# Performance work log

Measured on AMD Instinct MI355X. Metric: run time of the kernel, lower is better.

The kernel has to match this reference:

```python
import math
import jax, jax.numpy as jnp
import numpy as np

B_, H_, L_, N_ = 64, 256, 1024, 64  # batch, n_feat, n_embd(=seq len), complex state modes (d_state=128 -> 64 conj pairs)


def setup_inputs() -> dict:
    key = jax.random.key(0)
    ks = jax.random.split(key, 12)
    x = jax.random.normal(ks[0], (B_, H_, L_), jnp.float32)
    t = jax.random.randint(ks[1], (B_,), 0, 1000)
    # AdaLayerNorm linear: n_embd -> 2*n_embd
    ada_w = jax.random.normal(ks[2], (2 * L_, L_), jnp.float32) * 0.02
    ada_b = jnp.zeros((2 * L_,), jnp.float32)
    # S4Layer prenorm (LayerNorm over n_feat, affine)
    norm_w = jnp.ones((H_,), jnp.float32)
    norm_b = jnp.zeros((H_,), jnp.float32)
    # S4D-style diagonal SSM parameters
    log_dt = math.log(0.001) + jax.random.uniform(ks[3], (H_,), jnp.float32) * (math.log(0.1) - math.log(0.001))
    A_re = jnp.full((H_, N_), math.log(0.5), jnp.float32)            # A_real = -exp(A_re) = -0.5
    A_im = jnp.ones((H_, 1), jnp.float32) * (math.pi * jnp.arange(N_, dtype=jnp.float32))[None, :]
    C_re = jax.random.normal(ks[4], (2, H_, N_), jnp.float32) * (N_ ** -0.5)  # 2 channels: bidirectional
    C_im = jax.random.normal(ks[5], (2, H_, N_), jnp.float32) * (N_ ** -0.5)
    D = jax.random.normal(ks[6], (H_,), jnp.float32)
    out_w = jax.random.normal(ks[7], (H_, H_), jnp.float32) * (H_ ** -0.5)   # S4 output 1x1 conv
    out_b = jnp.zeros((H_,), jnp.float32)
    lin1_w = jax.random.normal(ks[8], (H_, H_), jnp.float32) * (H_ ** -0.5)
    lin1_b = jnp.zeros((H_,), jnp.float32)
    lin2_w = jax.random.normal(ks[9], (H_, H_), jnp.float32) * (H_ ** -0.5)
    lin2_b = jnp.zeros((H_,), jnp.float32)
    return dict(x=x, t=t, ada_w=ada_w, ada_b=ada_b, norm_w=norm_w, norm_b=norm_b,
                log_dt=log_dt, A_re=A_re, A_im=A_im, C_re=C_re, C_im=C_im, D=D,
                out_w=out_w, out_b=out_b, lin1_w=lin1_w, lin1_b=lin1_b,
                lin2_w=lin2_w, lin2_b=lin2_b)


def _ln(v):
    m = v.mean(-1, keepdims=True)
    s = v.var(-1, keepdims=True)
    return (v - m) * jax.lax.rsqrt(s + 1e-5)


def _forward(t, x, ada_w, ada_b, norm_w, norm_b, log_dt, A_re, A_im, C_re, C_im, D,
             out_w, out_b, lin1_w, lin1_b, lin2_w, lin2_b):
    B, H, L = x.shape
    # ---- AdaLayerNorm over last dim (n_embd = L) ----
    half = L // 2
    freqs = jnp.exp(jnp.arange(half, dtype=jnp.float32) * (-math.log(10000.0) / (half - 1)))
    emb = t.astype(jnp.float32)[:, None] * freqs[None, :]
    emb = jnp.concatenate([jnp.sin(emb), jnp.cos(emb)], axis=-1)           # (B, L)
    emb = jax.nn.silu(emb) @ ada_w.T + ada_b                                # (B, 2L)
    scale, shift = jnp.split(emb[:, None, :], 2, axis=2)                    # (B,1,L)
    x = _ln(x) * (1.0 + scale) + shift                                      # (B,H,L)
    # ---- S4Layer: prenorm over channels ----
    z = (_ln(x.transpose(0, 2, 1)) * norm_w + norm_b).transpose(0, 2, 1)    # (B,H,L)
    # ---- S4 (diagonal SSM) bidirectional FFT convolution ----
    dt = jnp.exp(log_dt)                                                    # (H,)
    A = -jnp.exp(A_re) + 1j * A_im                                          # (H,N)
    dtA = dt[:, None] * A
    dA = jnp.exp(dtA)
    C = (C_re + 1j * C_im) * ((dA - 1.0) / A)                               # ZOH-discretized (2,H,N)
    vand = jnp.exp(dtA[:, :, None] * jnp.arange(L, dtype=jnp.float32))      # (H,N,L)
    K = 2.0 * jnp.real(jnp.einsum('chn,hnl->chl', C, vand))                 # (2,H,L)
    k = jnp.pad(K[0], ((0, 0), (0, L))) + jnp.pad(K[1][:, ::-1], ((0, 0), (L, 0)))  # (H,2L)
    n = 2 * L
    y = jnp.fft.irfft(jnp.fft.rfft(z, n=n) * jnp.fft.rfft(k, n=n), n=n)[..., :L]
    y = y + D[:, None] * z
    y = jax.nn.gelu(y, approximate=False)
    y = jnp.einsum('oi,bil->bol', out_w, y) + out_b[None, :, None]          # S4 output 1x1 conv
    x2 = y + x                                                              # residual
    # ---- gated output ----
    g = jnp.tanh(x2) * jax.nn.sigmoid(x2)
    out1 = jnp.einsum('oi,bil->bol', lin1_w, g) + lin1_b[None, :, None] + x
    out2 = jnp.einsum('oi,bil->bol', lin2_w, g) + lin2_b[None, :, None]
    return (out1, out2)


def reference(x, t, ada_w, ada_b, norm_w, norm_b, log_dt, A_re, A_im, C_re, C_im, D,
              out_w, out_b, lin1_w, lin1_b, lin2_w, lin2_b):
    return _forward(t, x, ada_w, ada_b, norm_w, norm_b, log_dt, A_re, A_im, C_re, C_im,
                    D, out_w, out_b, lin1_w, lin1_b, lin2_w, lin2_b)
```

## Files before the change

kernel.cpp:

```cpp
#include <hip/hip_runtime.h>
#include <math.h>

#define Bq 64
#define Hq 256
#define Lq 1024
#define HLq (Hq*Lq)
#define BHLq (Bq*Hq*Lq)
#define HNq (Hq*64)

typedef __attribute__((ext_vector_type(8))) short bf16x8;
typedef __attribute__((ext_vector_type(4))) float f32x4;

__device__ __forceinline__ float sigmoidf_(float x){ return 1.f/(1.f+expf(-x)); }
__device__ __forceinline__ unsigned short f2bf(float f){
  unsigned u = __float_as_uint(f);
  u += 0x7FFF + ((u>>16)&1);
  return (unsigned short)(u>>16);
}
__device__ __forceinline__ float bf2f(unsigned short h){ return __uint_as_float(((unsigned)h)<<16); }

__global__ __launch_bounds__(256) void k_ada2(const int* __restrict__ tptr,
        const float* __restrict__ ada_w, float* __restrict__ Part){
  __shared__ float Es[64][68];
  __shared__ float Ws[64][68];
  const int tid = threadIdx.x;
  const int o0 = blockIdx.x * 64;
  const int kc = blockIdx.y;
  const int k0 = kc * 64;
  const float ci = -logf(10000.f) / 511.f;
  #pragma unroll
  for (int it = 0; it < 4; ++it){
    int fidx = it*256 + tid;
    int row = fidx >> 4;
    int c4  = fidx & 15;
    float tb = (float)tptr[row];
    float4 v;
    float* vp = &v.x;
    #pragma unroll
    for (int q = 0; q < 4; ++q){
      int k = k0 + c4*4 + q;
      float f = expf(ci * (float)(k & 511));
      float arg = tb * f;
      float s = (k < 512) ? sinf(arg) : cosf(arg);
      vp[q] = s * sigmoidf_(s);
    }
    *(float4*)&Es[row][c4*4] = v;
  }
  #pragma unroll
  for (int it = 0; it < 4; ++it){
    int fidx = it*256 + tid;
    int row = fidx >> 4;
    int c4  = fidx & 15;
    *(float4*)&Ws[row][c4*4] = *(const float4*)(ada_w + (size_t)(o0+row)*1024 + k0 + c4*4);
  }
  __syncthreads();
  float acc[4][4] = {};
  #pragma unroll
  for (int ks = 0; ks < 16; ++ks){
    int k = ks*4;
    float4 ev[4], wv[4];
    #pragma unroll
    for (int i=0;i<4;++i) ev[i] = *(const float4*)&Es[(tid>>4) + 16*i][k];
    #pragma unroll
    for (int j=0;j<4;++j) wv[j] = *(const float4*)&Ws[(tid&15) + 16*j][k];
    #pragma unroll
    for (int i=0;i<4;++i)
      #pragma unroll
      for (int j=0;j<4;++j)
        acc[i][j] += ev[i].x*wv[j].x + ev[i].y*wv[j].y + ev[i].z*wv[j].z + ev[i].w*wv[j].w;
  }
  float* pbase = Part + (size_t)kc*131072 + o0;
  #pragma unroll
  for (int i=0;i<4;++i){
    int b = (tid>>4) + 16*i;
    #pragma unroll
    for (int j=0;j<4;++j){
      int o = (tid&15) + 16*j;
      pbase[(size_t)b*2048 + o] = acc[i][j];
    }
  }
}

__global__ void k_red(const float* __restrict__ Part, const float* __restrict__ ada_b,
                      float* __restrict__ scsh){
  int idx = blockIdx.x*256 + threadIdx.x;
  float4 s = ((const float4*)ada_b)[idx & 511];
  #pragma unroll
  for (int p = 0; p < 16; ++p){
    float4 u = ((const float4*)Part)[p*32768 + idx];
    s.x += u.x; s.y += u.y; s.z += u.z; s.w += u.w;
  }
  ((float4*)scsh)[idx] = s;
}

__global__ void k_adaln(const float* __restrict__ x, const float* __restrict__ scsh,
                        float* __restrict__ A){
  const int bid = blockIdx.x;
  const int b = bid >> 8;
  const int tid = threadIdx.x;
  const float4* row = (const float4*)(x + (size_t)bid*1024);
  float4 v = row[tid];
  float s = v.x+v.y+v.z+v.w;
  float ss = v.x*v.x+v.y*v.y+v.z*v.z+v.w*v.w;
  #pragma unroll
  for (int off=32; off; off>>=1){ s += __shfl_xor(s,off); ss += __shfl_xor(ss,off); }
  __shared__ float rs_[4], rss_[4];
  int lane = tid & 63, w = tid >> 6;
  if (!lane){ rs_[w]=s; rss_[w]=ss; }
  __syncthreads();
  s  = rs_[0]+rs_[1]+rs_[2]+rs_[3];
  ss = rss_[0]+rss_[1]+rss_[2]+rss_[3];
  float mean = s * (1.f/1024.f);
  float var  = ss*(1.f/1024.f) - mean*mean;
  float rstd = rsqrtf(var + 1e-5f);
  float4 sc = ((const float4*)(scsh + b*2048))[tid];
  float4 sh = ((const float4*)(scsh + b*2048 + 1024))[tid];
  float4 o;
  o.x = (v.x-mean)*rstd*(1.f+sc.x) + sh.x;
  o.y = (v.y-mean)*rstd*(1.f+sc.y) + sh.y;
  o.z = (v.z-mean)*rstd*(1.f+sc.z) + sh.z;
  o.w = (v.w-mean)*rstd*(1.f+sc.w) + sh.w;
  ((float4*)(A + (size_t)bid*1024))[tid] = o;
}

__global__ void k_chln(const float* __restrict__ A, const float* __restrict__ nw,
                       const float* __restrict__ nb, unsigned short* __restrict__ Zb){
  const int b = blockIdx.y;
  const int l = blockIdx.x*256 + threadIdx.x;
  const float* base = A + (size_t)b*HLq + l;
  float s=0.f, ss=0.f;
  for (int h=0; h<256; ++h){ float v = base[h*1024]; s+=v; ss+=v*v; }
  float mean = s*(1.f/256.f);
  float var  = ss*(1.f/256.f) - mean*mean;
  float rstd = rsqrtf(var+1e-5f);
  unsigned short* zb = Zb + (size_t)b*HLq + l;
  for (int h=0; h<256; ++h){
    float v = base[h*1024];
    zb[h*1024] = f2bf((v-mean)*rstd*nw[h] + nb[h]);
  }
}

__global__ void k_ssmk(const float* __restrict__ log_dt, const float* __restrict__ A_re,
                       const float* __restrict__ A_im, const float* __restrict__ C_re,
                       const float* __restrict__ C_im, float* __restrict__ Kbuf){
  const int h = blockIdx.y;
  const int tid = threadIdx.x;
  __shared__ float dre[64], dim_[64], c0r[64], c0i[64], c1r[64], c1i[64];
  if (tid < 64){
    int n = tid;
    float dt = expf(log_dt[h]);
    float Ar = -expf(A_re[h*64+n]);
    float Ai = A_im[h*64+n];
    float dr = dt*Ar, di = dt*Ai;
    float er = expf(dr);
    float dAr = er*cosf(di), dAi = er*sinf(di);
    float den = Ar*Ar + Ai*Ai;
    float nr = dAr - 1.f, ni = dAi;
    float qr = (nr*Ar + ni*Ai)/den;
    float qi = (ni*Ar - nr*Ai)/den;
    float C0r = C_re[h*64+n],       C0i = C_im[h*64+n];
    float C1r = C_re[HNq + h*64+n], C1i = C_im[HNq + h*64+n];
    c0r[n] = C0r*qr - C0i*qi; c0i[n] = C0r*qi + C0i*qr;
    c1r[n] = C1r*qr - C1i*qi; c1i[n] = C1r*qi + C1i*qr;
    dre[n] = dr; dim_[n] = di;
  }
  __syncthreads();
  int l = blockIdx.x*256 + tid;
  float lf = (float)l;
  float a0=0.f, a1=0.f;
  for (int n=0;n<64;++n){
    float e  = expf(lf*dre[n]);
    float ph = lf*dim_[n];
    float wr = e*cosf(ph), wi = e*sinf(ph);
    a0 += c0r[n]*wr - c0i[n]*wi;
    a1 += c1r[n]*wr - c1i[n]*wi;
  }
  Kbuf[h*1024 + l]       = 2.f*a0;
  Kbuf[HLq + h*1024 + l] = 2.f*a1;
}

__global__ __launch_bounds__(256,2) void k_conv(const unsigned short* __restrict__ Zb,
        const float* __restrict__ Kbuf, const float* __restrict__ Dp,
        unsigned short* __restrict__ Cb){
  __shared__ unsigned short kcopy[8][2056];
  __shared__ unsigned short As[64][136];
  const int tid = threadIdx.x;
  const int h  = blockIdx.y;
  const int l0 = blockIdx.x * 512;
  const float* K0 = Kbuf + h*1024;
  const float* K1 = Kbuf + HLq + h*1024;
  for (int idx = tid; idx < 8*2056; idx += 256){
    int s = idx / 2056;
    int i = idx - s*2056;
    int q = 2046 - i - s;
    float v = 0.f;
    if (q >= 0) v = (q >= 1023) ? K0[q-1023] : K1[1022-q];
    kcopy[s][i] = f2bf(v);
  }
  const int lane = tid & 63;
  const int w    = tid >> 6;
  const int ln   = lane & 15;
  const int quad = lane >> 4;
  int kofs[8];
  #pragma unroll
  for (int nt=0; nt<8; ++nt){
    int l = l0 + w*128 + nt*16 + ln;
    int d = 1023 - l;
    int s = d & 7;
    kofs[nt] = s*2056 + (d - s) + quad*8;
  }
  const unsigned short* kbase = &kcopy[0][0];
  f32x4 acc[4][8] = {};
  for (int c = 0; c < 8; ++c){
    __syncthreads();
    #pragma unroll
    for (int pass = 0; pass < 4; ++pass){
      int b = pass*16 + (tid>>4);
      int col = (tid & 15)*8;
      *(uint4*)&As[b][col] = *(const uint4*)(Zb + ((size_t)b*256 + h)*1024 + c*128 + col);
    }
    __syncthreads();
    #pragma unroll
    for (int ks = 0; ks < 4; ++ks){
      int kk = ks*32 + quad*8;
      bf16x8 af[4];
      #pragma unroll
      for (int mt=0; mt<4; ++mt) af[mt] = *(const bf16x8*)&As[mt*16+ln][kk];
      int jb = c*128 + ks*32;
      bf16x8 bv[8];
      #pragma unroll
      for (int nt=0; nt<8; ++nt) bv[nt] = *(const bf16x8*)(kbase + kofs[nt] + jb);
      #pragma unroll
      for (int mt=0; mt<4; ++mt)
        #pragma unroll
        for (int nt=0; nt<8; ++nt)
          acc[mt][nt] = __builtin_amdgcn_mfma_f32_16x16x32_bf16(af[mt], bv[nt], acc[mt][nt], 0,0,0);
    }
  }
  float Dh = Dp[h];
  #pragma unroll
  for (int mt=0; mt<4; ++mt){
    #pragma unroll
    for (int reg=0; reg<4; ++reg){
      int b = mt*16 + quad*4 + reg;
      const unsigned short* zrow = Zb + ((size_t)b*256+h)*1024;
      unsigned short* crow = Cb + ((size_t)b*256+h)*1024;
      #pragma unroll
      for (int nt=0; nt<8; ++nt){
        int l = l0 + w*128 + nt*16 + ln;
        float y = acc[mt][nt][reg] + Dh*bf2f(zrow[l]);
        float g = 0.5f*y*(1.f + erff(y*0.70710678118f));
        crow[l] = f2bf(g);
      }
    }
  }
}

__global__ __launch_bounds__(256,2) void k_gate(const unsigned short* __restrict__ U,
        const float* __restrict__ W, const float* __restrict__ bias,
        const float* __restrict__ Ax, unsigned short* __restrict__ G){
  __shared__ unsigned short Ws[64][72];
  __shared__ unsigned short Us[256][72];
  const int tid = threadIdx.x;
  const int l0 = blockIdx.x * 256;
  const int o0 = blockIdx.y * 64;
  const int b  = blockIdx.z;
  const int lane = tid & 63, w = tid>>6, ln = lane&15, quad = lane>>4;
  f32x4 acc[4][4] = {};
  for (int ch = 0; ch < 4; ++ch){
    int ic0 = ch*64;
    __syncthreads();
    {
      int o = tid & 63;
      int i = (tid >> 6) * 16;
      const float* wsrc = W + (size_t)(o0+o)*256 + ic0 + i;
      unsigned pk[8];
      #pragma unroll
      for (int r=0;r<8;++r) pk[r] = (unsigned)f2bf(wsrc[2*r]) | ((unsigned)f2bf(wsrc[2*r+1])<<16);
      uint4* dst = (uint4*)&Ws[o][i];
      dst[0] = make_uint4(pk[0],pk[1],pk[2],pk[3]);
      dst[1] = make_uint4(pk[4],pk[5],pk[6],pk[7]);
    }
    #pragma unroll
    for (int it = 0; it < 16; ++it){
      int i4 = (tid>>6) + 4*(it&3);
      int l  = (it>>2)*64 + (tid&63);
      const unsigned short* usrc = U + ((size_t)b*256 + ic0 + i4*4)*1024 + l0 + l;
      unsigned short e0 = usrc[0], e1 = usrc[1024], e2 = usrc[2048], e3 = usrc[3072];
      uint2 val; val.x = (unsigned)e0 | ((unsigned)e1<<16); val.y = (unsigned)e2 | ((unsigned)e3<<16);
      *(uint2*)&Us[l][i4*4] = val;
    }
    __syncthreads();
    #pragma unroll
    for (int ks = 0; ks < 2; ++ks){
      int kk = ks*32 + quad*8;
      bf16x8 af[4], bv[4];
      #pragma unroll
      for (int mt=0;mt<4;++mt) af[mt] = *(const bf16x8*)&Ws[mt*16+ln][kk];
      #pragma unroll
      for (int nt=0;nt<4;++nt) bv[nt] = *(const bf16x8*)&Us[w*64+nt*16+ln][kk];
      #pragma unroll
      for (int mt=0;mt<4;++mt)
        #pragma unroll
        for (int nt=0;nt<4;++nt)
          acc[mt][nt] = __builtin_amdgcn_mfma_f32_16x16x32_bf16(af[mt], bv[nt], acc[mt][nt],0,0,0);
    }
  }
  #pragma unroll
  for (int mt=0;mt<4;++mt){
    #pragma unroll
    for (int reg=0;reg<4;++reg){
      int o = o0 + mt*16 + quad*4 + reg;
      float bo = bias[o];
      const float* arow = Ax + ((size_t)b*256 + o)*1024;
      unsigned short* grow = G + ((size_t)b*256 + o)*1024;
      #pragma unroll
      for (int nt=0;nt<4;++nt){
        int l = l0 + w*64 + nt*16 + ln;
        float v = acc[mt][nt][reg] + bo + arow[l];
        float g = tanhf(v)*sigmoidf_(v);
        grow[l] = f2bf(g);
      }
    }
  }
}

__global__ __launch_bounds__(256,2) void k_out(const unsigned short* __restrict__ G,
        const float* __restrict__ W1, const float* __restrict__ b1,
        const float* __restrict__ W2, const float* __restrict__ b2,
        const float* __restrict__ Ax, float* __restrict__ out){
  __shared__ unsigned short W1s[64][72];
  __shared__ unsigned short W2s[64][72];
  __shared__ unsigned short Us[256][72];
  const int tid = threadIdx.x;
  const int l0 = blockIdx.x * 256;
  const int o0 = blockIdx.y * 64;
  const int b  = blockIdx.z;
  const int lane = tid & 63, w = tid>>6, ln = lane&15, quad = lane>>4;
  f32x4 acc1[4][4] = {};
  f32x4 acc2[4][4] = {};
  for (int ch = 0; ch < 4; ++ch){
    int ic0 = ch*64;
    __syncthreads();
    {
      int o = tid & 63;
      int i = (tid >> 6) * 16;
      const float* w1src = W1 + (size_t)(o0+o)*256 + ic0 + i;
      const float* w2src = W2 + (size_t)(o0+o)*256 + ic0 + i;
      unsigned pk[8];
      #pragma unroll
      for (int r=0;r<8;++r) pk[r] = (unsigned)f2bf(w1src[2*r]) | ((unsigned)f2bf(w1src[2*r+1])<<16);
      uint4* dst1 = (uint4*)&W1s[o][i];
      dst1[0] = make_uint4(pk[0],pk[1],pk[2],pk[3]);
      dst1[1] = make_uint4(pk[4],pk[5],pk[6],pk[7]);
      #pragma unroll
      for (int r=0;r<8;++r) pk[r] = (unsigned)f2bf(w2src[2*r]) | ((unsigned)f2bf(w2src[2*r+1])<<16);
      uint4* dst2 = (uint4*)&W2s[o][i];
      dst2[0] = make_uint4(pk[0],pk[1],pk[2],pk[3]);
      dst2[1] = make_uint4(pk[4],pk[5],pk[6],pk[7]);
    }
    #pragma unroll
    for (int it = 0; it < 16; ++it){
      int i4 = (tid>>6) + 4*(it&3);
      int l  = (it>>2)*64 + (tid&63);
      const unsigned short* usrc = G + ((size_t)b*256 + ic0 + i4*4)*1024 + l0 + l;
      unsigned short e0 = usrc[0], e1 = usrc[1024], e2 = usrc[2048], e3 = usrc[3072];
      uint2 val; val.x = (unsigned)e0 | ((unsigned)e1<<16); val.y = (unsigned)e2 | ((unsigned)e3<<16);
      *(uint2*)&Us[l][i4*4] = val;
    }
    __syncthreads();
    #pragma unroll
    for (int ks = 0; ks < 2; ++ks){
      int kk = ks*32 + quad*8;
      bf16x8 bv[4];
      #pragma unroll
      for (int nt=0;nt<4;++nt) bv[nt] = *(const bf16x8*)&Us[w*64+nt*16+ln][kk];
      #pragma unroll
      for (int mt=0;mt<4;++mt){
        bf16x8 a1 = *(const bf16x8*)&W1s[mt*16+ln][kk];
        #pragma unroll
        for (int nt=0;nt<4;++nt)
          acc1[mt][nt] = __builtin_amdgcn_mfma_f32_16x16x32_bf16(a1, bv[nt], acc1[mt][nt],0,0,0);
      }
      #pragma unroll
      for (int mt=0;mt<4;++mt){
        bf16x8 a2 = *(const bf16x8*)&W2s[mt*16+ln][kk];
        #pragma unroll
        for (int nt=0;nt<4;++nt)
          acc2[mt][nt] = __builtin_amdgcn_mfma_f32_16x16x32_bf16(a2, bv[nt], acc2[mt][nt],0,0,0);
      }
    }
  }
  #pragma unroll
  for (int mt=0;mt<4;++mt){
    #pragma unroll
    for (int reg=0;reg<4;++reg){
      int o = o0 + mt*16 + quad*4 + reg;
      float bo1 = b1[o], bo2 = b2[o];
      const float* arow = Ax + ((size_t)b*256 + o)*1024;
      float* o1row = out + ((size_t)b*256 + o)*1024;
      float* o2row = o1row + BHLq;
      #pragma unroll
      for (int nt=0;nt<4;++nt){
        int l = l0 + w*64 + nt*16 + ln;
        o1row[l] = acc1[mt][nt][reg] + bo1 + arow[l];
        o2row[l] = acc2[mt][nt][reg] + bo2;
      }
    }
  }
}

extern "C" void kernel_launch(void* const* d_in, const int* in_sizes, int n_in,
                              void* d_out, int out_size, void* d_ws, size_t ws_size,
                              hipStream_t stream){
  const float* x      = (const float*)d_in[0];
  const int*   t      = (const int*)  d_in[1];
  const float* ada_w  = (const float*)d_in[2];
  const float* ada_b  = (const float*)d_in[3];
  const float* norm_w = (const float*)d_in[4];
  const float* norm_b = (const float*)d_in[5];
  const float* log_dt = (const float*)d_in[6];
  const float* A_re   = (const float*)d_in[7];
  const float* A_im   = (const float*)d_in[8];
  const float* C_re   = (const float*)d_in[9];
  const float* C_im   = (const float*)d_in[10];
  const float* Dp     = (const float*)d_in[11];
  const float* out_w  = (const float*)d_in[12];
  const float* out_b  = (const float*)d_in[13];
  const float* lin1_w = (const float*)d_in[14];
  const float* lin1_b = (const float*)d_in[15];
  const float* lin2_w = (const float*)d_in[16];
  const float* lin2_b = (const float*)d_in[17];

  float* Ax            = (float*)d_ws;
  unsigned short* Zb   = (unsigned short*)(Ax + BHLq);
  unsigned short* Cb   = Zb + BHLq;
  float* Kbuf          = (float*)(Cb + BHLq);
  float* Part          = Kbuf + 2*HLq;
  float* scsh          = Part + 16*64*2048;
  unsigned short* Gb   = Zb;
  float* out           = (float*)d_out;

  k_ada2  <<<dim3(32, 16), 256, 0, stream>>>(t, ada_w, Part);
  k_red   <<<128, 256, 0, stream>>>(Part, ada_b, scsh);
  k_adaln <<<Bq*Hq, 256, 0, stream>>>(x, scsh, Ax);
  k_chln  <<<dim3(4, Bq), 256, 0, stream>>>(Ax, norm_w, norm_b, Zb);
  k_ssmk  <<<dim3(4, Hq), 256, 0, stream>>>(log_dt, A_re, A_im, C_re, C_im, Kbuf);
  k_conv  <<<dim3(2, Hq), 256, 0, stream>>>(Zb, Kbuf, Dp, Cb);
  k_gate  <<<dim3(4, 4, Bq), 256, 0, stream>>>(Cb, out_w, out_b, Ax, Gb);
  k_out   <<<dim3(4, 4, Bq), 256, 0, stream>>>(Gb, lin1_w, lin1_b, lin2_w, lin2_b, Ax, out);
}
```

Before: 532.1 us.

## Fuse gate and output 1x1 convs into one kernel with pre-converted bf16 weights

```diff
diff --git a/kernel.cpp b/kernel.cpp
--- a/kernel.cpp
+++ b/kernel.cpp
@@ -91,6 +91,18 @@
     s.x += u.x; s.y += u.y; s.z += u.z; s.w += u.w;
   }
   ((float4*)scsh)[idx] = s;
+}
+
+__global__ void k_wcvt(const float* __restrict__ w0, const float* __restrict__ w1,
+                       const float* __restrict__ w2, unsigned short* __restrict__ wb){
+  int idx = blockIdx.x*256 + threadIdx.x;
+  const float* src = (idx < 16384) ? w0 : ((idx < 32768) ? w1 : w2);
+  int loc = idx & 16383;
+  float4 v = ((const float4*)src)[loc];
+  uint2 pk;
+  pk.x = (unsigned)f2bf(v.x) | ((unsigned)f2bf(v.y)<<16);
+  pk.y = (unsigned)f2bf(v.z) | ((unsigned)f2bf(v.w)<<16);
+  ((uint2*)wb)[idx] = pk;
 }
 
 __global__ void k_adaln(const float* __restrict__ x, const float* __restrict__ scsh,
@@ -256,154 +268,106 @@
   }
 }
 
-__global__ __launch_bounds__(256,2) void k_gate(const unsigned short* __restrict__ U,
-        const float* __restrict__ W, const float* __restrict__ bias,
-        const float* __restrict__ Ax, unsigned short* __restrict__ G){
-  __shared__ unsigned short Ws[64][72];
-  __shared__ unsigned short Us[256][72];
+__global__ __launch_bounds__(512,2) void k_fuse(const unsigned short* __restrict__ U,
+        const unsigned short* __restrict__ Wob, const float* __restrict__ out_b,
+        const unsigned short* __restrict__ W1b, const float* __restrict__ b1,
+        const unsigned short* __restrict__ W2b, const float* __restrict__ b2,
+        const float* __restrict__ Ax, float* __restrict__ out){
+  __shared__ unsigned short Us[64][280];
+  __shared__ unsigned short Gs[64][280];
   const int tid = threadIdx.x;
-  const int l0 = blockIdx.x * 256;
-  const int o0 = blockIdx.y * 64;
-  const int b  = blockIdx.z;
-  const int lane = tid & 63, w = tid>>6, ln = lane&15, quad = lane>>4;
-  f32x4 acc[4][4] = {};
-  for (int ch = 0; ch < 4; ++ch){
-    int ic0 = ch*64;
-    __syncthreads();
-    {
-      int o = tid & 63;
-      int i = (tid >> 6) * 16;
-      const float* wsrc = W + (size_t)(o0+o)*256 + ic0 + i;
-      unsigned pk[8];
-      #pragma unroll
-      for (int r=0;r<8;++r) pk[r] = (unsigned)f2bf(wsrc[2*r]) | ((unsigned)f2bf(wsrc[2*r+1])<<16);
-      uint4* dst = (uint4*)&Ws[o][i];
-      dst[0] = make_uint4(pk[0],pk[1],pk[2],pk[3]);
-      dst[1] = make_uint4(pk[4],pk[5],pk[6],pk[7]);
-    }
-    #pragma unroll
-    for (int it = 0; it < 16; ++it){
-      int i4 = (tid>>6) + 4*(it&3);
-      int l  = (it>>2)*64 + (tid&63);
-      const unsigned short* usrc = U + ((size_t)b*256 + ic0 + i4*4)*1024 + l0 + l;
+  const int l0 = blockIdx.x * 64;
+  const int b  = blockIdx.y;
+  const int lane = tid & 63, w = tid >> 6, ln = lane & 15, quad = lane >> 4;
+  {
+    int l   = tid & 63;
+    int grp = tid >> 6;
+    #pragma unroll
+    for (int it = 0; it < 8; ++it){
+      int i4 = it*8 + grp;
+      const unsigned short* usrc = U + ((size_t)b*256 + i4*4)*1024 + l0 + l;
       unsigned short e0 = usrc[0], e1 = usrc[1024], e2 = usrc[2048], e3 = usrc[3072];
       uint2 val; val.x = (unsigned)e0 | ((unsigned)e1<<16); val.y = (unsigned)e2 | ((unsigned)e3<<16);
       *(uint2*)&Us[l][i4*4] = val;
     }
-    __syncthreads();
-    #pragma unroll
-    for (int ks = 0; ks < 2; ++ks){
-      int kk = ks*32 + quad*8;
-      bf16x8 af[4], bv[4];
-      #pragma unroll
-      for (int mt=0;mt<4;++mt) af[mt] = *(const bf16x8*)&Ws[mt*16+ln][kk];
-      #pragma unroll
-      for (int nt=0;nt<4;++nt) bv[nt] = *(const bf16x8*)&Us[w*64+nt*16+ln][kk];
-      #pragma unroll
-      for (int mt=0;mt<4;++mt)
-        #pragma unroll
-        for (int nt=0;nt<4;++nt)
-          acc[mt][nt] = __builtin_amdgcn_mfma_f32_16x16x32_bf16(af[mt], bv[nt], acc[mt][nt],0,0,0);
-    }
-  }
-  #pragma unroll
-  for (int mt=0;mt<4;++mt){
+  }
+  __syncthreads();
+  f32x4 acc[2][4] = {};
+  #pragma unroll
+  for (int ks = 0; ks < 8; ++ks){
+    int kk = ks*32 + quad*8;
+    bf16x8 af[2], bv[4];
+    #pragma unroll
+    for (int mt=0;mt<2;++mt) af[mt] = *(const bf16x8*)(Wob + (size_t)(w*32+mt*16+ln)*256 + kk);
+    #pragma unroll
+    for (int nt=0;nt<4;++nt) bv[nt] = *(const bf16x8*)&Us[nt*16+ln][kk];
+    #pragma unroll
+    for (int mt=0;mt<2;++mt)
+      #pragma unroll
+      for (int nt=0;nt<4;++nt)
+        acc[mt][nt] = __builtin_amdgcn_mfma_f32_16x16x32_bf16(af[mt], bv[nt], acc[mt][nt],0,0,0);
+  }
+  float axv[2][4][4];
+  #pragma unroll
+  for (int mt=0;mt<2;++mt){
     #pragma unroll
     for (int reg=0;reg<4;++reg){
-      int o = o0 + mt*16 + quad*4 + reg;
-      float bo = bias[o];
-      const float* arow = Ax + ((size_t)b*256 + o)*1024;
-      unsigned short* grow = G + ((size_t)b*256 + o)*1024;
+      int o = w*32 + mt*16 + quad*4 + reg;
+      float bo = out_b[o];
+      const float* arow = Ax + ((size_t)b*256 + o)*1024 + l0;
       #pragma unroll
       for (int nt=0;nt<4;++nt){
-        int l = l0 + w*64 + nt*16 + ln;
-        float v = acc[mt][nt][reg] + bo + arow[l];
-        float g = tanhf(v)*sigmoidf_(v);
-        grow[l] = f2bf(g);
+        int l = nt*16 + ln;
+        float a = arow[l];
+        axv[mt][nt][reg] = a;
+        float v = acc[mt][nt][reg] + bo + a;
+        acc[mt][nt][reg] = tanhf(v)*sigmoidf_(v);
       }
     }
   }
-}
-
-__global__ __launch_bounds__(256,2) void k_out(const unsigned short* __restrict__ G,
-        const float* __restrict__ W1, const float* __restrict__ b1,
-        const float* __restrict__ W2, const float* __restrict__ b2,
-        const float* __restrict__ Ax, float* __restrict__ out){
-  __shared__ unsigned short W1s[64][72];
-  __shared__ unsigned short W2s[64][72];
-  __shared__ unsigned short Us[256][72];
-  const int tid = threadIdx.x;
-  const int l0 = blockIdx.x * 256;
-  const int o0 = blockIdx.y * 64;
-  const int b  = blockIdx.z;
-  const int lane = tid & 63, w = tid>>6, ln = lane&15, quad = lane>>4;
-  f32x4 acc1[4][4] = {};
-  f32x4 acc2[4][4] = {};
-  for (int ch = 0; ch < 4; ++ch){
-    int ic0 = ch*64;
-    __syncthreads();
-    {
-      int o = tid & 63;
-      int i = (tid >> 6) * 16;
-      const float* w1src = W1 + (size_t)(o0+o)*256 + ic0 + i;
-      const float* w2src = W2 + (size_t)(o0+o)*256 + ic0 + i;
-      unsigned pk[8];
-      #pragma unroll
-      for (int r=0;r<8;++r) pk[r] = (unsigned)f2bf(w1src[2*r]) | ((unsigned)f2bf(w1src[2*r+1])<<16);
-      uint4* dst1 = (uint4*)&W1s[o][i];
-      dst1[0] = make_uint4(pk[0],pk[1],pk[2],pk[3]);
-      dst1[1] = make_uint4(pk[4],pk[5],pk[6],pk[7]);
-      #pragma unroll
-      for (int r=0;r<8;++r) pk[r] = (unsigned)f2bf(w2src[2*r]) | ((unsigned)f2bf(w2src[2*r+1])<<16);
-      uint4* dst2 = (uint4*)&W2s[o][i];
-      dst2[0] = make_uint4(pk[0],pk[1],pk[2],pk[3]);
-      dst2[1] = make_uint4(pk[4],pk[5],pk[6],pk[7]);
-    }
-    #pragma unroll
-    for (int it = 0; it < 16; ++it){
-      int i4 = (tid>>6) + 4*(it&3);
-      int l  = (it>>2)*64 + (tid&63);
-      const unsigned short* usrc = G + ((size_t)b*256 + ic0 + i4*4)*1024 + l0 + l;
-      unsigned short e0 = usrc[0], e1 = usrc[1024], e2 = usrc[2048], e3 = usrc[3072];
-      uint2 val; val.x = (unsigned)e0 | ((unsigned)e1<<16); val.y = (unsigned)e2 | ((unsigned)e3<<16);
-      *(uint2*)&Us[l][i4*4] = val;
-    }
-    __syncthreads();
-    #pragma unroll
-    for (int ks = 0; ks < 2; ++ks){
-      int kk = ks*32 + quad*8;
-      bf16x8 bv[4];
-      #pragma unroll
-      for (int nt=0;nt<4;++nt) bv[nt] = *(const bf16x8*)&Us[w*64+nt*16+ln][kk];
-      #pragma unroll
-      for (int mt=0;mt<4;++mt){
-        bf16x8 a1 = *(const bf16x8*)&W1s[mt*16+ln][kk];
-        #pragma unroll
-        for (int nt=0;nt<4;++nt)
-          acc1[mt][nt] = __builtin_amdgcn_mfma_f32_16x16x32_bf16(a1, bv[nt], acc1[mt][nt],0,0,0);
-      }
-      #pragma unroll
-      for (int mt=0;mt<4;++mt){
-        bf16x8 a2 = *(const bf16x8*)&W2s[mt*16+ln][kk];
-        #pragma unroll
-        for (int nt=0;nt<4;++nt)
-          acc2[mt][nt] = __builtin_amdgcn_mfma_f32_16x16x32_bf16(a2, bv[nt], acc2[mt][nt],0,0,0);
-      }
-    }
-  }
-  #pragma unroll
-  for (int mt=0;mt<4;++mt){
+  #pragma unroll
+  for (int mt=0;mt<2;++mt){
+    int ob = w*32 + mt*16 + quad*4;
+    #pragma unroll
+    for (int nt=0;nt<4;++nt){
+      uint2 pk;
+      pk.x = (unsigned)f2bf(acc[mt][nt][0]) | ((unsigned)f2bf(acc[mt][nt][1])<<16);
+      pk.y = (unsigned)f2bf(acc[mt][nt][2]) | ((unsigned)f2bf(acc[mt][nt][3])<<16);
+      *(uint2*)&Gs[nt*16+ln][ob] = pk;
+    }
+  }
+  __syncthreads();
+  f32x4 acc1[2][4] = {}, acc2[2][4] = {};
+  #pragma unroll
+  for (int ks = 0; ks < 8; ++ks){
+    int kk = ks*32 + quad*8;
+    bf16x8 bv[4];
+    #pragma unroll
+    for (int nt=0;nt<4;++nt) bv[nt] = *(const bf16x8*)&Gs[nt*16+ln][kk];
+    #pragma unroll
+    for (int mt=0;mt<2;++mt){
+      bf16x8 a1 = *(const bf16x8*)(W1b + (size_t)(w*32+mt*16+ln)*256 + kk);
+      #pragma unroll
+      for (int nt=0;nt<4;++nt)
+        acc1[mt][nt] = __builtin_amdgcn_mfma_f32_16x16x32_bf16(a1, bv[nt], acc1[mt][nt],0,0,0);
+      bf16x8 a2 = *(const bf16x8*)(W2b + (size_t)(w*32+mt*16+ln)*256 + kk);
+      #pragma unroll
+      for (int nt=0;nt<4;++nt)
+        acc2[mt][nt] = __builtin_amdgcn_mfma_f32_16x16x32_bf16(a2, bv[nt], acc2[mt][nt],0,0,0);
+    }
+  }
+  #pragma unroll
+  for (int mt=0;mt<2;++mt){
     #pragma unroll
     for (int reg=0;reg<4;++reg){
-      int o = o0 + mt*16 + quad*4 + reg;
+      int o = w*32 + mt*16 + quad*4 + reg;
       float bo1 = b1[o], bo2 = b2[o];
-      const float* arow = Ax + ((size_t)b*256 + o)*1024;
-      float* o1row = out + ((size_t)b*256 + o)*1024;
+      float* o1row = out + ((size_t)b*256 + o)*1024 + l0;
       float* o2row = o1row + BHLq;
       #pragma unroll
       for (int nt=0;nt<4;++nt){
-        int l = l0 + w*64 + nt*16 + ln;
-        o1row[l] = acc1[mt][nt][reg] + bo1 + arow[l];
+        int l = nt*16 + ln;
+        o1row[l] = acc1[mt][nt][reg] + bo1 + axv[mt][nt][reg];
         o2row[l] = acc2[mt][nt][reg] + bo2;
       }
     }
@@ -438,15 +402,16 @@
   float* Kbuf          = (float*)(Cb + BHLq);
   float* Part          = Kbuf + 2*HLq;
   float* scsh          = Part + 16*64*2048;
-  unsigned short* Gb   = Zb;
+  unsigned short* wb   = (unsigned short*)(scsh + 64*2048);
   float* out           = (float*)d_out;
 
+  k_wcvt  <<<192, 256, 0, stream>>>(out_w, lin1_w, lin2_w, wb);
   k_ada2  <<<dim3(32, 16), 256, 0, stream>>>(t, ada_w, Part);
   k_red   <<<128, 256, 0, stream>>>(Part, ada_b, scsh);
   k_adaln <<<Bq*Hq, 256, 0, stream>>>(x, scsh, Ax);
   k_chln  <<<dim3(4, Bq), 256, 0, stream>>>(Ax, norm_w, norm_b, Zb);
   k_ssmk  <<<dim3(4, Hq), 256, 0, stream>>>(log_dt, A_re, A_im, C_re, C_im, Kbuf);
   k_conv  <<<dim3(2, Hq), 256, 0, stream>>>(Zb, Kbuf, Dp, Cb);
-  k_gate  <<<dim3(4, 4, Bq), 256, 0, stream>>>(Cb, out_w, out_b, Ax, Gb);
-  k_out   <<<dim3(4, 4, Bq), 256, 0, stream>>>(Gb, lin1_w, lin1_b, lin2_w, lin2_b, Ax, out);
-}
+  k_fuse  <<<dim3(16, Bq), 512, 0, stream>>>(Cb, wb, out_b, wb + 65536, lin1_b,
+                                             wb + 131072, lin2_b, Ax, out);
+}
```

New measurement: 491.9 us. 7.6% less time.
